# Kernel tuning notes

Hardware: AMD Instinct MI355X
Metric: run time of the kernel (lower is better)

The kernel has to match this reference:

```python
import jax, jax.numpy as jnp
import numpy as np
import math

B, T, C, H = 4, 2048, 1024, 16

def setup_inputs() -> dict:
    key = jax.random.key(0)
    k1, k2, k3 = jax.random.split(key, 3)
    scale = 1.0 / math.sqrt(C)
    return {
        "x": jax.random.normal(k1, (B, T, C), dtype=jnp.float32),
        "w_attn": jax.random.normal(k2, (C, 3 * C), dtype=jnp.float32) * scale,
        "b_attn": jnp.zeros((3 * C,), dtype=jnp.float32),
        "w_proj": jax.random.normal(k3, (C, C), dtype=jnp.float32) * scale,
        "b_proj": jnp.zeros((C,), dtype=jnp.float32),
    }

def reference(x, w_attn, b_attn, w_proj, b_proj):
    Bq, Tq, Cq = x.shape
    hd = Cq // H  # head dim
    qkv = x @ w_attn + b_attn                       # [B,T,3C]
    q, k, v = jnp.split(qkv, 3, axis=-1)
    # [B,T,C] -> [B,H,T,hd]
    q = q.reshape(Bq, Tq, H, hd).transpose(0, 2, 1, 3)
    k = k.reshape(Bq, Tq, H, hd).transpose(0, 2, 1, 3)
    v = v.reshape(Bq, Tq, H, hd).transpose(0, 2, 1, 3)
    att = jnp.einsum('bhqd,bhkd->bhqk', q, k) * (1.0 / math.sqrt(hd))
    causal = jnp.tril(jnp.ones((Tq, Tq), dtype=bool))
    att = jnp.where(causal[None, None], att, -jnp.inf)
    att = jax.nn.softmax(att, axis=-1)              # dropout p=0 (eval)
    y = jnp.einsum('bhqk,bhkd->bhqd', att, v)       # [B,H,T,hd]
    y = y.transpose(0, 2, 1, 3).reshape(Bq, Tq, Cq)
    return y @ w_proj + b_proj
```

## Files before the change

### kernel.cpp

```cpp
#include <hip/hip_runtime.h>


#define T_SEQ 2048
#define NB 4
#define NH 16
#define CDIM 1024
#define HD 64
#define BH (NB * NH)
#define QSCALE 0.1803368801111204f

typedef float f32x4 __attribute__((ext_vector_type(4)));
typedef float f32x16 __attribute__((ext_vector_type(16)));
typedef __bf16 bf16x8 __attribute__((ext_vector_type(8)));
typedef unsigned short u16x8 __attribute__((ext_vector_type(8)));
typedef unsigned short u16x4 __attribute__((ext_vector_type(4)));

__device__ __forceinline__ unsigned short f2b(float f) {
    union { float f; unsigned u; } v; v.f = f;
    unsigned u = v.u;
    u += 0x7FFFu + ((u >> 16) & 1u);
    return (unsigned short)(u >> 16);
}

__device__ __forceinline__ f32x4 fzero4() {
    f32x4 z; z[0] = 0.f; z[1] = 0.f; z[2] = 0.f; z[3] = 0.f; return z;
}

__device__ __forceinline__ f32x16 mfma32(bf16x8 a, bf16x8 b, f32x16 c) {
    return __builtin_amdgcn_mfma_f32_32x32x16_bf16(a, b, c, 0, 0, 0);
}

__device__ __forceinline__ void gld16(const void* gp, void* lp) {
    __builtin_amdgcn_global_load_lds(
        (const __attribute__((address_space(1))) unsigned int*)gp,
        (__attribute__((address_space(3))) unsigned int*)lp, 16, 0, 0);
}

__global__ __launch_bounds__(256) void cast_f32_bf16_kernel(
        const float* __restrict__ in, unsigned short* __restrict__ out, int n8) {
    int i = blockIdx.x * 256 + threadIdx.x;
    int stride = gridDim.x * 256;
    for (; i < n8; i += stride) {
        const float4* p = reinterpret_cast<const float4*>(in) + (size_t)i * 2;
        float4 a = p[0], b = p[1];
        u16x8 o;
        o[0] = f2b(a.x); o[1] = f2b(a.y); o[2] = f2b(a.z); o[3] = f2b(a.w);
        o[4] = f2b(b.x); o[5] = f2b(b.y); o[6] = f2b(b.z); o[7] = f2b(b.w);
        *(reinterpret_cast<u16x8*>(out) + i) = o;
    }
}

__global__ __launch_bounds__(256) void transpose_cast_kernel(
        const float* __restrict__ in, unsigned short* __restrict__ out, int R, int C) {
    __shared__ unsigned short tile[32][33];
    int tx = threadIdx.x, ty = threadIdx.y;
    int c0 = blockIdx.x * 32, r0 = blockIdx.y * 32;
    for (int rr = ty; rr < 32; rr += 8)
        tile[rr][tx] = f2b(in[(size_t)(r0 + rr) * C + c0 + tx]);
    __syncthreads();
    for (int rr = ty; rr < 32; rr += 8)
        out[(size_t)(c0 + rr) * R + r0 + tx] = tile[tx][rr];
}

template <int EPI>
__global__ __launch_bounds__(256) void gemm_bt_kernel(
        const unsigned short* __restrict__ A, const unsigned short* __restrict__ Bt,
        const float* __restrict__ bias, float* __restrict__ outF,
        unsigned short* __restrict__ q_out, unsigned short* __restrict__ k_out,
        unsigned short* __restrict__ v_out, int M, int N, int K) {
    __shared__ alignas(16) unsigned short As[128][32];
    __shared__ alignas(16) unsigned short Bs[128][32];

    int tid = threadIdx.x;
    int wid = tid >> 6, lane = tid & 63;
    int g = lane >> 4, lc = lane & 15;
    int wr = (wid >> 1) * 64, wc = (wid & 1) * 64;
    int m0 = blockIdx.y * 128, n0 = blockIdx.x * 128;

    f32x4 acc[4][4];
#pragma unroll
    for (int m = 0; m < 4; ++m)
#pragma unroll
        for (int n = 0; n < 4; ++n) acc[m][n] = fzero4();

    int srow = tid >> 2;
    int scol = (tid & 3) * 8;
    const unsigned short* Ap = A + (size_t)(m0 + srow) * K + scol;
    const unsigned short* Bp = Bt + (size_t)(n0 + srow) * K + scol;
    unsigned short* lA0 = &As[wid * 16][0];
    unsigned short* lA1 = &As[64 + wid * 16][0];
    unsigned short* lB0 = &Bs[wid * 16][0];
    unsigned short* lB1 = &Bs[64 + wid * 16][0];

    for (int k0 = 0; k0 < K; k0 += 32) {
        __syncthreads();
        gld16(Ap + k0, lA0);
        gld16(Ap + (size_t)64 * K + k0, lA1);
        gld16(Bp + k0, lB0);
        gld16(Bp + (size_t)64 * K + k0, lB1);
        __syncthreads();

        bf16x8 af[4], bfr[4];
#pragma unroll
        for (int m = 0; m < 4; ++m)
            af[m] = *(const bf16x8*)&As[wr + m * 16 + lc][g * 8];
#pragma unroll
        for (int n = 0; n < 4; ++n)
            bfr[n] = *(const bf16x8*)&Bs[wc + n * 16 + lc][g * 8];
#pragma unroll
        for (int m = 0; m < 4; ++m)
#pragma unroll
            for (int n = 0; n < 4; ++n)
                acc[m][n] = __builtin_amdgcn_mfma_f32_16x16x32_bf16(af[m], bfr[n], acc[m][n], 0, 0, 0);
    }

#pragma unroll
    for (int m = 0; m < 4; ++m) {
        int rowb = m0 + wr + m * 16 + g * 4;
#pragma unroll
        for (int n = 0; n < 4; ++n) {
            int col = n0 + wc + n * 16 + lc;
            float bv = bias[col];
            if (EPI == 0) {
#pragma unroll
                for (int i = 0; i < 4; ++i)
                    outF[(size_t)(rowb + i) * N + col] = acc[m][n][i] + bv;
            } else {
                int which = col >> 10;
                int c = col & 1023;
                int h = c >> 6, d = c & 63;
                int bh_ = (rowb >> 11) * NH + h;
                int tl = rowb & 2047;
                if (which == 2) {
                    u16x4 vq;
#pragma unroll
                    for (int i = 0; i < 4; ++i) vq[i] = f2b(acc[m][n][i] + bv);
                    *(u16x4*)&v_out[(size_t)bh_ * (HD * T_SEQ) + (size_t)d * T_SEQ + tl] = vq;
                } else {
                    unsigned short* dst = which ? k_out : q_out;
                    float sc = which ? 1.0f : QSCALE;
#pragma unroll
                    for (int i = 0; i < 4; ++i)
                        dst[((size_t)bh_ * T_SEQ + tl + i) * HD + d] =
                            f2b((acc[m][n][i] + bv) * sc);
                }
            }
        }
    }
}

__global__ __launch_bounds__(256) void attn32_kernel(
        const unsigned short* __restrict__ Qb, const unsigned short* __restrict__ Kb,
        const unsigned short* __restrict__ Vt, unsigned short* __restrict__ Yb) {
    __shared__ alignas(16) unsigned short Kl[64 * 64];
    __shared__ alignas(16) unsigned short Vl[64 * 64];

    int tid = threadIdx.x;
    int wid = tid >> 6, lane = tid & 63;
    int ql = lane & 31, hi = lane >> 5;
    int ql7 = ql & 7;

    int id = blockIdx.x;
    int swz = (id & 7) * 64 + (id >> 3);
    int bh = swz >> 3;
    int b8 = swz & 7;
    int p = b8 * 4 + wid;
    size_t hb = (size_t)bh * (T_SEQ * HD);

    int qA0 = p * 32, qB0 = (63 - p) * 32;
    int ktA = p >> 1;
    int ktB = 31 - (p >> 1);
    int nt = 32 - 2 * b8;
    { int alt = 2 * b8 + 2; if (alt > nt) nt = alt; }

    bf16x8 qB_[4];
    const unsigned short* QBp = Qb + hb + (size_t)(qB0 + ql) * HD + hi * 8;
#pragma unroll
    for (int d = 0; d < 4; ++d) qB_[d] = *(const bf16x8*)(QBp + d * 16);
    const unsigned short* QAp = Qb + hb + (size_t)(qA0 + ql) * HD + hi * 8;

    f32x16 zz;
#pragma unroll
    for (int r = 0; r < 16; ++r) zz[r] = 0.f;
    f32x16 oA0 = zz, oA1 = zz, oB0 = zz, oB1 = zz;
    float mA = -__builtin_inff(), lA = 0.f;
    float mB = -__builtin_inff(), lB = 0.f;

    int r8 = lane >> 3;
    int sslot = (lane & 7) ^ r8;
    const unsigned short* Kg = Kb + hb + (size_t)(wid * 16 + r8) * HD + sslot * 8;
    const unsigned short* Vg = Vt + hb + (size_t)(wid * 16 + r8) * T_SEQ + sslot * 8;
    char* KlB = (char*)Kl + wid * 2048;
    char* VlB = (char*)Vl + wid * 2048;

#define KF(K0, D) (*(const bf16x8*)&Kl[(((K0)*32 + ql) << 6) + ((((D)*2 + hi) ^ ql7) << 3)])
#define VF(DB, T) (*(const bf16x8*)&Vl[(((DB)*32 + ql) << 6) + ((((T)*2 + hi) ^ ql7) << 3)])

#define TILE(QF, O0, O1, MI, LI, Q0, DIAG)                                           \
    {                                                                                \
        f32x16 s0_, s1_;                                                             \
        __builtin_amdgcn_s_setprio(1);                                               \
        s0_ = mfma32(KF(0, 0), QF[0], zz);                                           \
        s0_ = mfma32(KF(0, 1), QF[1], s0_);                                          \
        s0_ = mfma32(KF(0, 2), QF[2], s0_);                                          \
        s0_ = mfma32(KF(0, 3), QF[3], s0_);                                          \
        s1_ = mfma32(KF(1, 0), QF[0], zz);                                           \
        s1_ = mfma32(KF(1, 1), QF[1], s1_);                                          \
        s1_ = mfma32(KF(1, 2), QF[2], s1_);                                          \
        s1_ = mfma32(KF(1, 3), QF[3], s1_);                                          \
        __builtin_amdgcn_s_setprio(0);                                               \
        if (DIAG) {                                                                  \
            int qg_ = (Q0) + ql;                                                     \
            _Pragma("unroll")                                                        \
            for (int r = 0; r < 16; ++r) {                                           \
                int kof_ = k0 + 8 * (r >> 2) + (r & 3) + 4 * hi;                     \
                if (kof_ > qg_) s0_[r] = -__builtin_inff();                          \
                if (kof_ + 32 > qg_) s1_[r] = -__builtin_inff();                     \
            }                                                                        \
        }                                                                            \
        float t_[8];                                                                 \
        _Pragma("unroll")                                                            \
        for (int r = 0; r < 8; ++r)                                                  \
            t_[r] = fmaxf(fmaxf(s0_[r], s0_[r + 8]), fmaxf(s1_[r], s1_[r + 8]));     \
        _Pragma("unroll")                                                            \
        for (int r = 0; r < 4; ++r) t_[r] = fmaxf(t_[r], t_[r + 4]);                 \
        float pm_ = fmaxf(fmaxf(t_[0], t_[1]), fmaxf(t_[2], t_[3]));                 \
        pm_ = fmaxf(pm_, __shfl_xor(pm_, 32));                                       \
        float mn_ = fmaxf(MI, pm_);                                                  \
        float f_ = __builtin_amdgcn_exp2f(MI - mn_);                                 \
        MI = mn_;                                                                    \
        _Pragma("unroll")                                                            \
        for (int r = 0; r < 16; ++r) {                                               \
            s0_[r] = __builtin_amdgcn_exp2f(s0_[r] - mn_);                           \
            s1_[r] = __builtin_amdgcn_exp2f(s1_[r] - mn_);                           \
        }                                                                            \
        float u_[8];                                                                 \
        _Pragma("unroll")                                                            \
        for (int r = 0; r < 8; ++r)                                                  \
            u_[r] = (s0_[r] + s0_[r + 8]) + (s1_[r] + s1_[r + 8]);                   \
        _Pragma("unroll")                                                            \
        for (int r = 0; r < 4; ++r) u_[r] += u_[r + 4];                              \
        float ps_ = (u_[0] + u_[1]) + (u_[2] + u_[3]);                               \
        ps_ += __shfl_xor(ps_, 32);                                                  \
        LI = LI * f_ + ps_;                                                          \
        O0 *= f_;                                                                    \
        O1 *= f_;                                                                    \
        unsigned pw_[16];                                                            \
        _Pragma("unroll")                                                            \
        for (int K0 = 0; K0 < 2; ++K0) {                                             \
            _Pragma("unroll")                                                        \
            for (int h2 = 0; h2 < 2; ++h2) {                                         \
                float e0_, e1_, e2_, e3_, e4_, e5_, e6_, e7_;                        \
                if (K0 == 0) {                                                       \
                    e0_ = s0_[8 * h2 + 0]; e1_ = s0_[8 * h2 + 1];                    \
                    e2_ = s0_[8 * h2 + 2]; e3_ = s0_[8 * h2 + 3];                    \
                    e4_ = s0_[8 * h2 + 4]; e5_ = s0_[8 * h2 + 5];                    \
                    e6_ = s0_[8 * h2 + 6]; e7_ = s0_[8 * h2 + 7];                    \
                } else {                                                             \
                    e0_ = s1_[8 * h2 + 0]; e1_ = s1_[8 * h2 + 1];                    \
                    e2_ = s1_[8 * h2 + 2]; e3_ = s1_[8 * h2 + 3];                    \
                    e4_ = s1_[8 * h2 + 4]; e5_ = s1_[8 * h2 + 5];                    \
                    e6_ = s1_[8 * h2 + 6]; e7_ = s1_[8 * h2 + 7];                    \
                }                                                                    \
                unsigned a_, b_, c_, d_;                                             \
                asm("v_cvt_pk_bf16_f32 %0, %1, %2" : "=v"(a_) : "v"(e0_), "v"(e1_)); \
                asm("v_cvt_pk_bf16_f32 %0, %1, %2" : "=v"(b_) : "v"(e2_), "v"(e3_)); \
                asm("v_cvt_pk_bf16_f32 %0, %1, %2" : "=v"(c_) : "v"(e4_), "v"(e5_)); \
                asm("v_cvt_pk_bf16_f32 %0, %1, %2" : "=v"(d_) : "v"(e6_), "v"(e7_)); \
                asm("v_permlane32_swap_b32 %0, %1" : "+v"(a_), "+v"(c_));            \
                asm("v_permlane32_swap_b32 %0, %1" : "+v"(b_), "+v"(d_));            \
                pw_[(K0 * 2 + h2) * 4 + 0] = a_;                                     \
                pw_[(K0 * 2 + h2) * 4 + 1] = b_;                                     \
                pw_[(K0 * 2 + h2) * 4 + 2] = c_;                                     \
                pw_[(K0 * 2 + h2) * 4 + 3] = d_;                                     \
            }                                                                        \
        }                                                                            \
        __builtin_amdgcn_s_setprio(1);                                               \
        _Pragma("unroll")                                                            \
        for (int t = 0; t < 4; ++t) {                                                \
            union { unsigned u[4]; bf16x8 v; } pf_;                                  \
            pf_.u[0] = pw_[t * 4 + 0]; pf_.u[1] = pw_[t * 4 + 1];                    \
            pf_.u[2] = pw_[t * 4 + 2]; pf_.u[3] = pw_[t * 4 + 3];                    \
            O0 = mfma32(VF(0, t), pf_.v, O0);                                        \
            O1 = mfma32(VF(1, t), pf_.v, O1);                                        \
        }                                                                            \
        __builtin_amdgcn_s_setprio(0);                                               \
    }

    for (int kt = 0; kt < nt; ++kt) {
        int k0 = kt * 64;
        __syncthreads();
        gld16(Kg + (size_t)k0 * HD, KlB);
        gld16(Kg + (size_t)(k0 + 8) * HD, KlB + 1024);
        gld16(Vg + k0, VlB);
        gld16(Vg + k0 + 8 * T_SEQ, VlB + 1024);
        __syncthreads();

        bool doA = (kt <= ktA);
        bf16x8 qA_[4];
        if (doA) {
#pragma unroll
            for (int d = 0; d < 4; ++d) qA_[d] = *(const bf16x8*)(QAp + d * 16);
        }
        if (kt <= ktB) TILE(qB_, oB0, oB1, mB, lB, qB0, kt == ktB);
        if (doA) TILE(qA_, oA0, oA1, mA, lA, qA0, kt == ktA);
    }
#undef TILE
#undef KF
#undef VF

    int bb = bh >> 4, h = bh & 15;
    float ivA = 1.0f / lA, ivB = 1.0f / lB;
#pragma unroll
    for (int dblk = 0; dblk < 2; ++dblk) {
#pragma unroll
        for (int a = 0; a < 4; ++a) {
            u16x4 wA, wB;
#pragma unroll
            for (int i = 0; i < 4; ++i) {
                float vA = (dblk ? oA1[4 * a + i] : oA0[4 * a + i]) * ivA;
                float vB = (dblk ? oB1[4 * a + i] : oB0[4 * a + i]) * ivB;
                wA[i] = f2b(vA);
                wB[i] = f2b(vB);
            }
            int dq = dblk * 32 + 8 * a + 4 * hi;
            *(u16x4*)&Yb[((size_t)(bb * T_SEQ + qA0 + ql)) * CDIM + h * HD + dq] = wA;
            *(u16x4*)&Yb[((size_t)(bb * T_SEQ + qB0 + ql)) * CDIM + h * HD + dq] = wB;
        }
    }
}

extern "C" void kernel_launch(void* const* d_in, const int* in_sizes, int n_in,
                              void* d_out, int out_size, void* d_ws, size_t ws_size,
                              hipStream_t stream) {
    const float* x      = (const float*)d_in[0];
    const float* w_attn = (const float*)d_in[1];
    const float* b_attn = (const float*)d_in[2];
    const float* w_proj = (const float*)d_in[3];
    const float* b_proj = (const float*)d_in[4];
    float* out = (float*)d_out;

    char* ws = (char*)d_ws;
    unsigned short* xb  = (unsigned short*)(ws);
    unsigned short* wTa = (unsigned short*)(ws + 16777216);
    unsigned short* wTp = (unsigned short*)(ws + 23068672);
    unsigned short* qb  = (unsigned short*)(ws + 25165824);
    unsigned short* kb  = (unsigned short*)(ws + 41943040);
    unsigned short* vTb = (unsigned short*)(ws + 58720256);
    unsigned short* yb  = xb;

    cast_f32_bf16_kernel<<<2048, 256, 0, stream>>>(x, xb, (NB * T_SEQ * CDIM) / 8);
    transpose_cast_kernel<<<dim3(3072 / 32, 1024 / 32), dim3(32, 8), 0, stream>>>(
        w_attn, wTa, 1024, 3072);
    transpose_cast_kernel<<<dim3(1024 / 32, 1024 / 32), dim3(32, 8), 0, stream>>>(
        w_proj, wTp, 1024, 1024);

    gemm_bt_kernel<1><<<dim3(3072 / 128, 8192 / 128), 256, 0, stream>>>(
        xb, wTa, b_attn, nullptr, qb, kb, vTb, 8192, 3072, 1024);

    attn32_kernel<<<dim3(512), 256, 0, stream>>>(qb, kb, vTb, yb);

    gemm_bt_kernel<0><<<dim3(1024 / 128, 8192 / 128), 256, 0, stream>>>(
        yb, wTp, b_proj, out, nullptr, nullptr, nullptr, 8192, 1024, 1024);
}
```

Baseline: 195.8 us.

## Double-buffer GEMM and attention loads, split KV tiles across 8 waves with merge

The GEMM now double-buffers its LDS tiles so the next K-slice loads while MFMAs run, with one barrier per iteration. The attention kernel moves to 512 threads: two wave halves take alternating KV tiles for the same query rows, and their partial softmax states are merged through LDS at the end. K/V tiles are double-buffered, the online-softmax rescale is skipped while the running max grows by at most 8, and the PV MFMAs are interleaved with the bf16 packing. The changes add a merge pass, more LDS and more registers per block, and the lazy rescale relies on fp32 headroom for exp values up to 2^8.

```diff
diff --git a/kernel.cpp b/kernel.cpp
--- a/kernel.cpp
+++ b/kernel.cpp
@@ -68,8 +68,8 @@
         const float* __restrict__ bias, float* __restrict__ outF,
         unsigned short* __restrict__ q_out, unsigned short* __restrict__ k_out,
         unsigned short* __restrict__ v_out, int M, int N, int K) {
-    __shared__ alignas(16) unsigned short As[128][32];
-    __shared__ alignas(16) unsigned short Bs[128][32];
+    __shared__ alignas(16) unsigned short As[2][128 * 32];
+    __shared__ alignas(16) unsigned short Bs[2][128 * 32];
 
     int tid = threadIdx.x;
     int wid = tid >> 6, lane = tid & 63;
@@ -87,32 +87,39 @@
     int scol = (tid & 3) * 8;
     const unsigned short* Ap = A + (size_t)(m0 + srow) * K + scol;
     const unsigned short* Bp = Bt + (size_t)(n0 + srow) * K + scol;
-    unsigned short* lA0 = &As[wid * 16][0];
-    unsigned short* lA1 = &As[64 + wid * 16][0];
-    unsigned short* lB0 = &Bs[wid * 16][0];
-    unsigned short* lB1 = &Bs[64 + wid * 16][0];
-
-    for (int k0 = 0; k0 < K; k0 += 32) {
-        __syncthreads();
-        gld16(Ap + k0, lA0);
-        gld16(Ap + (size_t)64 * K + k0, lA1);
-        gld16(Bp + k0, lB0);
-        gld16(Bp + (size_t)64 * K + k0, lB1);
-        __syncthreads();
+    int ldst = (wid * 16) * 32;
+    int ldst2 = (64 + wid * 16) * 32;
+
+#define GSTAGE(BUF, KOFF)                                      \
+    gld16(Ap + (KOFF), &As[BUF][ldst]);                        \
+    gld16(Ap + (size_t)64 * K + (KOFF), &As[BUF][ldst2]);      \
+    gld16(Bp + (KOFF), &Bs[BUF][ldst]);                        \
+    gld16(Bp + (size_t)64 * K + (KOFF), &Bs[BUF][ldst2]);
+
+    GSTAGE(0, 0)
+    __syncthreads();
+
+    int nk = K >> 5;
+    for (int it = 0; it < nk; ++it) {
+        int cur = it & 1;
+        if (it + 1 < nk) { GSTAGE(cur ^ 1, (it + 1) << 5) }
 
         bf16x8 af[4], bfr[4];
 #pragma unroll
         for (int m = 0; m < 4; ++m)
-            af[m] = *(const bf16x8*)&As[wr + m * 16 + lc][g * 8];
+            af[m] = *(const bf16x8*)&As[cur][(wr + m * 16 + lc) * 32 + g * 8];
 #pragma unroll
         for (int n = 0; n < 4; ++n)
-            bfr[n] = *(const bf16x8*)&Bs[wc + n * 16 + lc][g * 8];
+            bfr[n] = *(const bf16x8*)&Bs[cur][(wc + n * 16 + lc) * 32 + g * 8];
 #pragma unroll
         for (int m = 0; m < 4; ++m)
 #pragma unroll
             for (int n = 0; n < 4; ++n)
                 acc[m][n] = __builtin_amdgcn_mfma_f32_16x16x32_bf16(af[m], bfr[n], acc[m][n], 0, 0, 0);
-    }
+
+        __syncthreads();
+    }
+#undef GSTAGE
 
 #pragma unroll
     for (int m = 0; m < 4; ++m) {
@@ -149,29 +156,28 @@
     }
 }
 
-__global__ __launch_bounds__(256) void attn32_kernel(
+__global__ __launch_bounds__(512, 4) void attn32_kernel(
         const unsigned short* __restrict__ Qb, const unsigned short* __restrict__ Kb,
         const unsigned short* __restrict__ Vt, unsigned short* __restrict__ Yb) {
-    __shared__ alignas(16) unsigned short Kl[64 * 64];
-    __shared__ alignas(16) unsigned short Vl[64 * 64];
+    __shared__ alignas(16) char smem[34816];
 
     int tid = threadIdx.x;
     int wid = tid >> 6, lane = tid & 63;
     int ql = lane & 31, hi = lane >> 5;
     int ql7 = ql & 7;
+    int pi = wid & 3, hf = wid >> 2;
 
     int id = blockIdx.x;
     int swz = (id & 7) * 64 + (id >> 3);
     int bh = swz >> 3;
     int b8 = swz & 7;
-    int p = b8 * 4 + wid;
+    int p = b8 * 4 + pi;
     size_t hb = (size_t)bh * (T_SEQ * HD);
 
     int qA0 = p * 32, qB0 = (63 - p) * 32;
     int ktA = p >> 1;
     int ktB = 31 - (p >> 1);
     int nt = 32 - 2 * b8;
-    { int alt = 2 * b8 + 2; if (alt > nt) nt = alt; }
 
     bf16x8 qB_[4];
     const unsigned short* QBp = Qb + hb + (size_t)(qB0 + ql) * HD + hi * 8;
@@ -187,14 +193,16 @@
     float mB = -__builtin_inff(), lB = 0.f;
 
     int r8 = lane >> 3;
-    int sslot = (lane & 7) ^ r8;
-    const unsigned short* Kg = Kb + hb + (size_t)(wid * 16 + r8) * HD + sslot * 8;
-    const unsigned short* Vg = Vt + hb + (size_t)(wid * 16 + r8) * T_SEQ + sslot * 8;
-    char* KlB = (char*)Kl + wid * 2048;
-    char* VlB = (char*)Vl + wid * 2048;
-
-#define KF(K0, D) (*(const bf16x8*)&Kl[(((K0)*32 + ql) << 6) + ((((D)*2 + hi) ^ ql7) << 3)])
-#define VF(DB, T) (*(const bf16x8*)&Vl[(((DB)*32 + ql) << 6) + ((((T)*2 + hi) ^ ql7) << 3)])
+    int sslot8 = ((lane & 7) ^ r8) * 8;
+    const unsigned short* Kg = Kb + hb + (size_t)(wid * 8 + r8) * HD + sslot8;
+    const unsigned short* Vg = Vt + hb + (size_t)(wid * 8 + r8) * T_SEQ + sslot8;
+
+    gld16(Kg, smem + wid * 1024);
+    gld16(Vg, smem + 8192 + wid * 1024);
+    __syncthreads();
+
+#define KF(K0, D) (*(const bf16x8*)&KB_[(((K0)*32 + ql) << 6) + ((((D)*2 + hi) ^ ql7) << 3)])
+#define VF(DB, T) (*(const bf16x8*)&VB_[(((DB)*32 + ql) << 6) + ((((T)*2 + hi) ^ ql7) << 3)])
 
 #define TILE(QF, O0, O1, MI, LI, Q0, DIAG)                                           \
     {                                                                                \
@@ -226,9 +234,15 @@
         for (int r = 0; r < 4; ++r) t_[r] = fmaxf(t_[r], t_[r + 4]);                 \
         float pm_ = fmaxf(fmaxf(t_[0], t_[1]), fmaxf(t_[2], t_[3]));                 \
         pm_ = fmaxf(pm_, __shfl_xor(pm_, 32));                                       \
-        float mn_ = fmaxf(MI, pm_);                                                  \
-        float f_ = __builtin_amdgcn_exp2f(MI - mn_);                                 \
-        MI = mn_;                                                                    \
+        float mn_ = MI;                                                              \
+        if (!__all((int)(pm_ <= MI + 8.f))) {   \
+            mn_ = fmaxf(MI, pm_);                                                    \
+            float f_ = __builtin_amdgcn_exp2f(MI - mn_);                             \
+            MI = mn_;                                                                \
+            LI *= f_;                                                                \
+            O0 *= f_;                                                                \
+            O1 *= f_;                                                                \
+        }                                                                            \
         _Pragma("unroll")                                                            \
         for (int r = 0; r < 16; ++r) {                                               \
             s0_[r] = __builtin_amdgcn_exp2f(s0_[r] - mn_);                           \
@@ -242,26 +256,19 @@
         for (int r = 0; r < 4; ++r) u_[r] += u_[r + 4];                              \
         float ps_ = (u_[0] + u_[1]) + (u_[2] + u_[3]);                               \
         ps_ += __shfl_xor(ps_, 32);                                                  \
-        LI = LI * f_ + ps_;                                                          \
-        O0 *= f_;                                                                    \
-        O1 *= f_;                                                                    \
-        unsigned pw_[16];                                                            \
-        _Pragma("unroll")                                                            \
-        for (int K0 = 0; K0 < 2; ++K0) {                                             \
+        LI += ps_;                                                                   \
+        _Pragma("unroll")                                                            \
+        for (int K0_ = 0; K0_ < 2; ++K0_) {                                          \
             _Pragma("unroll")                                                        \
-            for (int h2 = 0; h2 < 2; ++h2) {                                         \
-                float e0_, e1_, e2_, e3_, e4_, e5_, e6_, e7_;                        \
-                if (K0 == 0) {                                                       \
-                    e0_ = s0_[8 * h2 + 0]; e1_ = s0_[8 * h2 + 1];                    \
-                    e2_ = s0_[8 * h2 + 2]; e3_ = s0_[8 * h2 + 3];                    \
-                    e4_ = s0_[8 * h2 + 4]; e5_ = s0_[8 * h2 + 5];                    \
-                    e6_ = s0_[8 * h2 + 6]; e7_ = s0_[8 * h2 + 7];                    \
-                } else {                                                             \
-                    e0_ = s1_[8 * h2 + 0]; e1_ = s1_[8 * h2 + 1];                    \
-                    e2_ = s1_[8 * h2 + 2]; e3_ = s1_[8 * h2 + 3];                    \
-                    e4_ = s1_[8 * h2 + 4]; e5_ = s1_[8 * h2 + 5];                    \
-                    e6_ = s1_[8 * h2 + 6]; e7_ = s1_[8 * h2 + 7];                    \
-                }                                                                    \
+            for (int h2_ = 0; h2_ < 2; ++h2_) {                                      \
+                float e0_ = K0_ ? s1_[8 * h2_ + 0] : s0_[8 * h2_ + 0];               \
+                float e1_ = K0_ ? s1_[8 * h2_ + 1] : s0_[8 * h2_ + 1];               \
+                float e2_ = K0_ ? s1_[8 * h2_ + 2] : s0_[8 * h2_ + 2];               \
+                float e3_ = K0_ ? s1_[8 * h2_ + 3] : s0_[8 * h2_ + 3];               \
+                float e4_ = K0_ ? s1_[8 * h2_ + 4] : s0_[8 * h2_ + 4];               \
+                float e5_ = K0_ ? s1_[8 * h2_ + 5] : s0_[8 * h2_ + 5];               \
+                float e6_ = K0_ ? s1_[8 * h2_ + 6] : s0_[8 * h2_ + 6];               \
+                float e7_ = K0_ ? s1_[8 * h2_ + 7] : s0_[8 * h2_ + 7];               \
                 unsigned a_, b_, c_, d_;                                             \
                 asm("v_cvt_pk_bf16_f32 %0, %1, %2" : "=v"(a_) : "v"(e0_), "v"(e1_)); \
                 asm("v_cvt_pk_bf16_f32 %0, %1, %2" : "=v"(b_) : "v"(e2_), "v"(e3_)); \
@@ -269,63 +276,102 @@
                 asm("v_cvt_pk_bf16_f32 %0, %1, %2" : "=v"(d_) : "v"(e6_), "v"(e7_)); \
                 asm("v_permlane32_swap_b32 %0, %1" : "+v"(a_), "+v"(c_));            \
                 asm("v_permlane32_swap_b32 %0, %1" : "+v"(b_), "+v"(d_));            \
-                pw_[(K0 * 2 + h2) * 4 + 0] = a_;                                     \
-                pw_[(K0 * 2 + h2) * 4 + 1] = b_;                                     \
-                pw_[(K0 * 2 + h2) * 4 + 2] = c_;                                     \
-                pw_[(K0 * 2 + h2) * 4 + 3] = d_;                                     \
+                union { unsigned u[4]; bf16x8 v; } pf_;                              \
+                pf_.u[0] = a_; pf_.u[1] = b_; pf_.u[2] = c_; pf_.u[3] = d_;          \
+                __builtin_amdgcn_s_setprio(1);                                       \
+                O0 = mfma32(VF(0, K0_ * 2 + h2_), pf_.v, O0);                        \
+                O1 = mfma32(VF(1, K0_ * 2 + h2_), pf_.v, O1);                        \
+                __builtin_amdgcn_s_setprio(0);                                       \
             }                                                                        \
         }                                                                            \
-        __builtin_amdgcn_s_setprio(1);                                               \
-        _Pragma("unroll")                                                            \
-        for (int t = 0; t < 4; ++t) {                                                \
-            union { unsigned u[4]; bf16x8 v; } pf_;                                  \
-            pf_.u[0] = pw_[t * 4 + 0]; pf_.u[1] = pw_[t * 4 + 1];                    \
-            pf_.u[2] = pw_[t * 4 + 2]; pf_.u[3] = pw_[t * 4 + 3];                    \
-            O0 = mfma32(VF(0, t), pf_.v, O0);                                        \
-            O1 = mfma32(VF(1, t), pf_.v, O1);                                        \
-        }                                                                            \
-        __builtin_amdgcn_s_setprio(0);                                               \
     }
 
     for (int kt = 0; kt < nt; ++kt) {
+        int cur = kt & 1;
         int k0 = kt * 64;
+        if (kt + 1 < nt) {
+            int nb = cur ^ 1;
+            gld16(Kg + (size_t)(kt + 1) * 64 * HD, smem + nb * 16384 + wid * 1024);
+            gld16(Vg + (kt + 1) * 64, smem + nb * 16384 + 8192 + wid * 1024);
+        }
+        const unsigned short* KB_ = (const unsigned short*)(smem + cur * 16384);
+        const unsigned short* VB_ = (const unsigned short*)(smem + cur * 16384 + 8192);
+        if ((kt & 1) == hf) {
+            if (kt <= ktB) TILE(qB_, oB0, oB1, mB, lB, qB0, kt == ktB);
+            if (kt <= ktA) {
+                bf16x8 qA_[4];
+#pragma unroll
+                for (int d = 0; d < 4; ++d) qA_[d] = *(const bf16x8*)(QAp + d * 16);
+                TILE(qA_, oA0, oA1, mA, lA, qA0, kt == ktA);
+            }
+        }
         __syncthreads();
-        gld16(Kg + (size_t)k0 * HD, KlB);
-        gld16(Kg + (size_t)(k0 + 8) * HD, KlB + 1024);
-        gld16(Vg + k0, VlB);
-        gld16(Vg + k0 + 8 * T_SEQ, VlB + 1024);
-        __syncthreads();
-
-        bool doA = (kt <= ktA);
-        bf16x8 qA_[4];
-        if (doA) {
-#pragma unroll
-            for (int d = 0; d < 4; ++d) qA_[d] = *(const bf16x8*)(QAp + d * 16);
-        }
-        if (kt <= ktB) TILE(qB_, oB0, oB1, mB, lB, qB0, kt == ktB);
-        if (doA) TILE(qA_, oA0, oA1, mA, lA, qA0, kt == ktA);
     }
 #undef TILE
 #undef KF
 #undef VF
 
+    float* mrg = (float*)smem;
     int bb = bh >> 4, h = bh & 15;
-    float ivA = 1.0f / lA, ivB = 1.0f / lB;
-#pragma unroll
-    for (int dblk = 0; dblk < 2; ++dblk) {
-#pragma unroll
-        for (int a = 0; a < 4; ++a) {
-            u16x4 wA, wB;
-#pragma unroll
-            for (int i = 0; i < 4; ++i) {
-                float vA = (dblk ? oA1[4 * a + i] : oA0[4 * a + i]) * ivA;
-                float vB = (dblk ? oB1[4 * a + i] : oB0[4 * a + i]) * ivB;
-                wA[i] = f2b(vA);
-                wB[i] = f2b(vB);
+    for (int rr = 0; rr < 2; ++rr) {
+        __syncthreads();
+        if ((pi >> 1) == rr && hf == 1) {
+            float* s0 = mrg + (((pi & 1) * 2 + 0) * 64 + lane) * 34;
+            float* s1 = mrg + (((pi & 1) * 2 + 1) * 64 + lane) * 34;
+#pragma unroll
+            for (int x = 0; x < 16; ++x) {
+                s0[x] = oA0[x]; s0[16 + x] = oA1[x];
+                s1[x] = oB0[x]; s1[16 + x] = oB1[x];
             }
-            int dq = dblk * 32 + 8 * a + 4 * hi;
-            *(u16x4*)&Yb[((size_t)(bb * T_SEQ + qA0 + ql)) * CDIM + h * HD + dq] = wA;
-            *(u16x4*)&Yb[((size_t)(bb * T_SEQ + qB0 + ql)) * CDIM + h * HD + dq] = wB;
+            s0[32] = mA; s0[33] = lA;
+            s1[32] = mB; s1[33] = lB;
+        }
+        __syncthreads();
+        if ((pi >> 1) == rr && hf == 0) {
+            const float* s0 = mrg + (((pi & 1) * 2 + 0) * 64 + lane) * 34;
+            const float* s1 = mrg + (((pi & 1) * 2 + 1) * 64 + lane) * 34;
+            {
+                float m1 = s0[32], l1 = s0[33];
+                float mm = fmaxf(mA, m1);
+                float c0 = __builtin_amdgcn_exp2f(mA - mm);
+                float c1 = __builtin_amdgcn_exp2f(m1 - mm);
+                float iv = 1.f / (lA * c0 + l1 * c1);
+#pragma unroll
+                for (int dblk = 0; dblk < 2; ++dblk)
+#pragma unroll
+                    for (int a = 0; a < 4; ++a) {
+                        u16x4 wv;
+#pragma unroll
+                        for (int i = 0; i < 4; ++i) {
+                            float v = ((dblk ? oA1[4 * a + i] : oA0[4 * a + i]) * c0 +
+                                       s0[dblk * 16 + 4 * a + i] * c1) * iv;
+                            wv[i] = f2b(v);
+                        }
+                        int dq = dblk * 32 + 8 * a + 4 * hi;
+                        *(u16x4*)&Yb[((size_t)(bb * T_SEQ + qA0 + ql)) * CDIM + h * HD + dq] = wv;
+                    }
+            }
+            {
+                float m1 = s1[32], l1 = s1[33];
+                float mm = fmaxf(mB, m1);
+                float c0 = __builtin_amdgcn_exp2f(mB - mm);
+                float c1 = __builtin_amdgcn_exp2f(m1 - mm);
+                float iv = 1.f / (lB * c0 + l1 * c1);
+#pragma unroll
+                for (int dblk = 0; dblk < 2; ++dblk)
+#pragma unroll
+                    for (int a = 0; a < 4; ++a) {
+                        u16x4 wv;
+#pragma unroll
+                        for (int i = 0; i < 4; ++i) {
+                            float v = ((dblk ? oB1[4 * a + i] : oB0[4 * a + i]) * c0 +
+                                       s1[dblk * 16 + 4 * a + i] * c1) * iv;
+                            wv[i] = f2b(v);
+                        }
+                        int dq = dblk * 32 + 8 * a + 4 * hi;
+                        *(u16x4*)&Yb[((size_t)(bb * T_SEQ + qB0 + ql)) * CDIM + h * HD + dq] = wv;
+                    }
+            }
         }
     }
 }
@@ -358,7 +404,7 @@
     gemm_bt_kernel<1><<<dim3(3072 / 128, 8192 / 128), 256, 0, stream>>>(
         xb, wTa, b_attn, nullptr, qb, kb, vTb, 8192, 3072, 1024);
 
-    attn32_kernel<<<dim3(512), 256, 0, stream>>>(qb, kb, vTb, yb);
+    attn32_kernel<<<dim3(512), 512, 0, stream>>>(qb, kb, vTb, yb);
 
     gemm_bt_kernel<0><<<dim3(1024 / 128, 8192 / 128), 256, 0, stream>>>(
         yb, wTp, b_proj, out, nullptr, nullptr, nullptr, 8192, 1024, 1024);
```

Result: slower. 267.1 us (+36.4%).
